# Kernel tuning notes

Hardware: AMD Instinct MI355X
Metric: run time of the kernel (lower is better)

Reference implementation:

```python
import jax, jax.numpy as jnp
from jax import lax
import numpy as np

B, S = 64, 16
GD, LD, PD, HD, CD = 64, 32, 8, 64, 64  # global, local, periodic, hidden, coder dims
TWO_PI = 6.283185307179586


def _conv(x, w, b):
    y = lax.conv_general_dilated(x, w, (2, 2), [(1, 1), (1, 1)])
    return y + b[None, :, None, None]


def _deconv(x, w, b):
    # torch ConvTranspose2d(k=4, s=2, p=1); w is [in, out, 4, 4].
    # Equivalent: dilate lhs by 2, pad k-1-p=2 each side, conv with flipped kernel.
    wt = jnp.flip(w, (2, 3)).transpose(1, 0, 2, 3)  # -> OIHW
    y = lax.conv_general_dilated(x, wt, (1, 1), [(2, 2), (2, 2)], lhs_dilation=(2, 2))
    return y + b[None, :, None, None]


def _bn(x, g, b, eps=1e-5):
    # training-mode BatchNorm2d (biased variance, per-channel affine)
    m = x.mean((0, 2, 3), keepdims=True)
    v = x.var((0, 2, 3), keepdims=True)
    return (x - m) * lax.rsqrt(v + eps) * g[None, :, None, None] + b[None, :, None, None]


def setup_inputs() -> dict:
    key = jax.random.key(0)
    ks = iter(jax.random.split(key, 40))
    n = lambda shape, s=0.02: jax.random.normal(next(ks), shape, jnp.float32) * s
    return {
        "Z_l": jax.random.normal(next(ks), (B, LD, S, S), jnp.float32),
        "Z_g": jax.random.normal(next(ks), (B, GD, S, S), jnp.float32),
        "imgs": jax.random.normal(next(ks), (B, 3, 128, 128), jnp.float32),
        "phi": jax.random.uniform(next(ks), (B, PD, 1, 1), jnp.float32),
        "lW": n((HD, GD)), "lb": n((HD,)),
        "l1W": n((PD, HD)), "l1b": n((PD,)),
        "l2W": n((PD, HD)), "l2b": n((PD,)),
        "cod_w0": n((64, 3, 4, 4)), "cod_b0": n((64,)),
        "cod_g0": 1.0 + n((64,)), "cod_be0": n((64,)),
        "cod_w1": n((128, 64, 4, 4)), "cod_b1": n((128,)),
        "cod_g1": 1.0 + n((128,)), "cod_be1": n((128,)),
        "cod_w2": n((CD, 128, 4, 4)), "cod_b2": n((CD,)),
        "gen_w0": n((CD + LD + GD + PD, 256, 4, 4)), "gen_b0": n((256,)),
        "gen_g0": 1.0 + n((256,)), "gen_be0": n((256,)),
        "gen_w1": n((256, 128, 4, 4)), "gen_b1": n((128,)),
        "gen_g1": 1.0 + n((128,)), "gen_be1": n((128,)),
        "gen_w2": n((128, 3, 4, 4)), "gen_b2": n((3,)),
    }


def reference(Z_l, Z_g, imgs, phi, lW, lb, l1W, l1b, l2W, l2b,
              cod_w0, cod_b0, cod_g0, cod_be0, cod_w1, cod_b1, cod_g1, cod_be1,
              cod_w2, cod_b2,
              gen_w0, gen_b0, gen_g0, gen_be0, gen_w1, gen_b1, gen_g1, gen_be1,
              gen_w2, gen_b2):
    # --- image coder: [B,3,128,128] -> [B,CD,16,16] ---
    h = jax.nn.leaky_relu(_bn(_conv(imgs, cod_w0, cod_b0), cod_g0, cod_be0), 0.2)
    h = jax.nn.leaky_relu(_bn(_conv(h, cod_w1, cod_b1), cod_g1, cod_be1), 0.2)
    Z_c = jnp.tanh(_conv(h, cod_w2, cod_b2))
    # --- periodic noise: vectorized outer-product replacing S*S python loop ---
    zg = Z_g[:, :, 0, 0]                       # [B, GD]
    x = jax.nn.relu(zg @ lW.T + lb)            # [B, HD]
    K1 = x @ l1W.T + l1b                       # [B, PD]
    K2 = x @ l2W.T + l2b                       # [B, PD]
    idx = jnp.arange(S, dtype=jnp.float32)
    wave = K1[:, :, None, None] * idx[:, None] + K2[:, :, None, None] * idx[None, :]
    Z_p = jnp.sin(wave + phi * TWO_PI)         # [B, PD, S, S]
    # --- generator ---
    Z = jnp.concatenate((Z_c, Z_l, Z_g, Z_p), axis=1)  # [B, 168, 16, 16]
    h = jax.nn.relu(_bn(_deconv(Z, gen_w0, gen_b0), gen_g0, gen_be0))
    h = jax.nn.relu(_bn(_deconv(h, gen_w1, gen_b1), gen_g1, gen_be1))
    return jnp.tanh(_deconv(h, gen_w2, gen_b2))        # [B, 3, 128, 128]
```

## Files before the change

kernel.cpp:

```cpp
#include <hip/hip_runtime.h>
#include <hip/hip_bf16.h>

#define TWO_PI_F 6.2831853071795864769f

typedef __attribute__((ext_vector_type(8))) __bf16 bf16x8;
typedef __attribute__((ext_vector_type(4))) float f32x4;

__device__ __forceinline__ float bf2f_raw(unsigned short u) {
    return __uint_as_float(((unsigned int)u) << 16);
}
__device__ __forceinline__ unsigned short f2bf(float f) {
    unsigned int u = __float_as_uint(f);
    unsigned int r = (u + 0x7FFFu + ((u >> 16) & 1u)) >> 16;
    return (unsigned short)r;
}
__device__ __forceinline__ float loadIn(const void* p, size_t i, bool f32) {
    return f32 ? ((const float*)p)[i] : bf2f_raw(((const unsigned short*)p)[i]);
}

__device__ __forceinline__ uint4 bn_fuse8(uint4 v, const float* __restrict__ sc,
                                          const float* __restrict__ sh, int c0, float slope) {
    unsigned short us[8];
    *(uint4*)us = v;
#pragma unroll
    for (int k = 0; k < 8; ++k) {
        float f = bf2f_raw(us[k]) * sc[c0 + k] + sh[c0 + k];
        f = f > 0.f ? f : slope * f;
        us[k] = f2bf(f);
    }
    return *(const uint4*)us;
}

static constexpr size_t OFF_WC0 = 0;
static constexpr size_t OFF_WG2 = 3072;
static constexpr size_t OFF_P   = 9216;
static constexpr size_t OFF_CB0 = OFF_P + 0;
static constexpr size_t OFF_CG0 = OFF_P + 64;
static constexpr size_t OFF_CBE0= OFF_P + 128;
static constexpr size_t OFF_CB1 = OFF_P + 192;
static constexpr size_t OFF_CG1 = OFF_P + 320;
static constexpr size_t OFF_CBE1= OFF_P + 448;
static constexpr size_t OFF_CB2 = OFF_P + 576;
static constexpr size_t OFF_GB0 = OFF_P + 640;
static constexpr size_t OFF_GG0 = OFF_P + 896;
static constexpr size_t OFF_GBE0= OFF_P + 1152;
static constexpr size_t OFF_GB1 = OFF_P + 1408;
static constexpr size_t OFF_GG1 = OFF_P + 1536;
static constexpr size_t OFF_GBE1= OFF_P + 1664;
static constexpr size_t OFF_GB2 = OFF_P + 1792;
static constexpr size_t OFF_SSUM  = OFF_P + 2048;
static constexpr size_t OFF_SSQ   = OFF_SSUM + 576;
static constexpr size_t OFF_SCALE = OFF_SSUM + 1152;
static constexpr size_t OFF_SHIFT = OFF_SCALE + 576;
static constexpr size_t OFF_K12   = OFF_SHIFT + 576;
static constexpr size_t OFF_FLAG  = OFF_K12 + 1024;
static constexpr size_t FP32_END  = OFF_FLAG + 16;
static constexpr size_t UXT = 2 * FP32_END;
static constexpr size_t UYT = UXT + 16777216;
static constexpr size_t UZT = UYT + 8388608;
static constexpr size_t UW0 = UYT + 33554432;
static constexpr size_t UW1 = UW0 + 786432;
static constexpr size_t UWC1 = UW1 + 524288;
static constexpr size_t UWC2 = UWC1 + 131072;
static constexpr size_t UW2 = UWC2 + 131072;
static constexpr size_t WS_END_USHORT = UW2 + 32768;
static constexpr size_t WS_NEED_BYTES = WS_END_USHORT * 2;


__global__ void detect_kernel(const unsigned short* __restrict__ imgs, int* __restrict__ flag) {
    int t = threadIdx.x;
    unsigned short u = imgs[t];
    int e = (u >> 7) & 0xFF;
    unsigned long long b = __ballot(e >= 0xC0);
    __shared__ int cnt[4];
    if ((t & 63) == 0) cnt[t >> 6] = __popcll(b);
    __syncthreads();
    if (t == 0) flag[0] = (cnt[0] + cnt[1] + cnt[2] + cnt[3] >= 4) ? 1 : 0;
}

struct CvtJobs {
    const void* src[16];
    float* dst[16];
    int off[17];
};

__global__ void cvt_all_kernel(CvtJobs J, int total, const int* __restrict__ flg) {
    int i = blockIdx.x * 256 + threadIdx.x;
    if (i >= total) return;
    bool f32 = flg[0] != 0;
    int k = 0;
#pragma unroll
    for (int t = 0; t < 15; ++t) { if (i >= J.off[t + 1]) k = t + 1; }
    int r = i - J.off[k];
    J.dst[k][r] = loadIn(J.src[k], r, f32);
}

__global__ void zero_kernel(float* p, int n) {
    int i = blockIdx.x * 256 + threadIdx.x;
    if (i < n) p[i] = 0.f;
}

__global__ void pack_w2_kernel(const void* __restrict__ src, unsigned short* __restrict__ dst,
                               int ICreal, int ICP, int OC, const int* __restrict__ flg) {
    bool f32 = flg[0] != 0;
    int i = blockIdx.x * 256 + threadIdx.x;
    int total = 16 * OC * ICP;
    if (i >= total) return;
    int jj = i & 7;
    int lane = (i >> 3) & 63;
    int j = (i >> 9) & 3;
    int t3 = i >> 11;
    int NK = ICP / 32;
    int kc = t3 % NK;
    int t4 = t3 / NK;
    int NOCT = OC / 64;
    int oct = t4 % NOCT;
    int ktap = t4 / NOCT;
    int kq = lane >> 4, n = lane & 15;
    int ic = kc * 32 + kq * 8 + jj;
    int oc = oct * 64 + n * 4 + j;
    unsigned short v = 0;
    if (ic < ICreal) v = f2bf(loadIn(src, ((size_t)(ic * OC + oc) << 4) + ktap, f32));
    dst[i] = v;
}

__global__ void pack_w2s_kernel(const void* __restrict__ src, unsigned short* __restrict__ dst,
                                int ICP, int OCreal, const int* __restrict__ flg) {
    bool f32 = flg[0] != 0;
    int i = blockIdx.x * 256 + threadIdx.x;
    int NK = ICP / 32;
    int total = 16 * NK * 512;
    if (i >= total) return;
    int jj = i & 7;
    int lane = (i >> 3) & 63;
    int t3 = i >> 9;
    int kc = t3 % NK;
    int ktap = t3 / NK;
    int kq = lane >> 4, n = lane & 15;
    int ic = kc * 32 + kq * 8 + jj;
    unsigned short v = 0;
    if (n < OCreal) v = f2bf(loadIn(src, ((size_t)(ic * OCreal + n) << 4) + ktap, f32));
    dst[i] = v;
}

__global__ void pack_wc_kernel(const void* __restrict__ src, unsigned short* __restrict__ dst,
                               int IC, int OC, const int* __restrict__ flg) {
    bool f32 = flg[0] != 0;
    int i = blockIdx.x * 256 + threadIdx.x;
    int total = 16 * OC * IC;
    if (i >= total) return;
    int jj = i & 7;
    int lane = (i >> 3) & 63;
    int j = (i >> 9) & 3;
    int t3 = i >> 11;
    int NK = IC / 32;
    int kc = t3 % NK;
    int t4 = t3 / NK;
    int NOCT = OC / 64;
    int oct = t4 % NOCT;
    int ktap = t4 / NOCT;
    int kq = lane >> 4, n = lane & 15;
    int ic = kc * 32 + kq * 8 + jj;
    int oc = oct * 64 + j * 16 + n;
    dst[i] = f2bf(loadIn(src, ((size_t)(oc * IC + ic) << 4) + ktap, f32));
}

__global__ void mlp_kernel(const void* __restrict__ Zg,
                           const void* __restrict__ lW, const void* __restrict__ lb,
                           const void* __restrict__ l1W, const void* __restrict__ l1b,
                           const void* __restrict__ l2W, const void* __restrict__ l2b,
                           float* __restrict__ K12, const int* __restrict__ flg) {
    bool f32 = flg[0] != 0;
    int b = blockIdx.x;
    int t = threadIdx.x;
    __shared__ float xs[64];
    float acc = loadIn(lb, t, f32);
    for (int c = 0; c < 64; ++c)
        acc += loadIn(Zg, (size_t)(b * 64 + c) * 256, f32) * loadIn(lW, t * 64 + c, f32);
    xs[t] = fmaxf(acc, 0.f);
    __syncthreads();
    if (t < 16) {
        int p = t & 7;
        const void* Wp = (t < 8) ? l1W : l2W;
        const void* bp = (t < 8) ? l1b : l2b;
        float a = loadIn(bp, p, f32);
        for (int h = 0; h < 64; ++h) a += xs[h] * loadIn(Wp, p * 64 + h, f32);
        K12[b * 16 + t] = a;
    }
}

__global__ void conv0_s2d_kernel(const void* __restrict__ imgs, const float* __restrict__ w,
                                 const float* __restrict__ bias, unsigned short* __restrict__ xs,
                                 const int* __restrict__ flg) {
    bool f32 = flg[0] != 0;
    int b = blockIdx.z;
    int tile = blockIdx.x;
    int Y0 = (tile >> 2) * 16, X0 = (tile & 3) * 16;
    __shared__ float vin[3 * 34 * 35];
    __shared__ float wl[64 * 49];
    for (int i = threadIdx.x; i < 3 * 34 * 34; i += 256) {
        int c = i % 34; int t = i / 34; int r = t % 34; int ic = t / 34;
        int iy = 2 * Y0 - 1 + r, ix = 2 * X0 - 1 + c;
        float v = 0.f;
        if (((unsigned)iy < 128u) & ((unsigned)ix < 128u))
            v = loadIn(imgs, ((size_t)(b * 3 + ic) * 128 + iy) * 128 + ix, f32);
        vin[(ic * 34 + r) * 35 + c] = v;
    }
    for (int i = threadIdx.x; i < 3072; i += 256) {
        int oc = i / 48, idx = i % 48;
        wl[oc * 49 + idx] = w[i];
    }
    __syncthreads();
    int q = threadIdx.x >> 2;
    int ocq = threadIdx.x & 3;
    int qy = q >> 3, qx = q & 7;
    float acc[4][16];
#pragma unroll
    for (int p = 0; p < 4; ++p)
#pragma unroll
        for (int o = 0; o < 16; ++o) acc[p][o] = 0.f;
    for (int ic = 0; ic < 3; ++ic) {
        float v[6][6];
#pragma unroll
        for (int r = 0; r < 6; ++r)
#pragma unroll
            for (int c = 0; c < 6; ++c)
                v[r][c] = vin[(ic * 34 + 4 * qy + r) * 35 + 4 * qx + c];
#pragma unroll
        for (int o = 0; o < 16; ++o) {
            const float* wo = wl + (ocq * 16 + o) * 49 + ic * 16;
#pragma unroll
            for (int ky = 0; ky < 4; ++ky)
#pragma unroll
                for (int kx = 0; kx < 4; ++kx) {
                    float wv = wo[ky * 4 + kx];
                    acc[0][o] = fmaf(v[ky][kx], wv, acc[0][o]);
                    acc[1][o] = fmaf(v[ky][kx + 2], wv, acc[1][o]);
                    acc[2][o] = fmaf(v[ky + 2][kx], wv, acc[2][o]);
                    acc[3][o] = fmaf(v[ky + 2][kx + 2], wv, acc[3][o]);
                }
        }
    }
    int j = (Y0 >> 1) + qy, i2 = (X0 >> 1) + qx;
#pragma unroll
    for (int p = 0; p < 4; ++p) {
        int dy = p >> 1, dx = p & 1;
        unsigned short tmp[16];
#pragma unroll
        for (int o = 0; o < 16; ++o) tmp[o] = f2bf(acc[p][o] + bias[ocq * 16 + o]);
        unsigned short* dst = xs + (((size_t)((b * 2 + dy) * 2 + dx) * 32 + j) * 32 + i2) * 64 + ocq * 16;
        *(uint4*)(dst) = *(const uint4*)(tmp);
        *(uint4*)(dst + 8) = *(const uint4*)(tmp + 8);
    }
}

__global__ void conv1_mfma_kernel(const unsigned short* __restrict__ xs,
                                  const unsigned short* __restrict__ wp,
                                  const float* __restrict__ bias,
                                  const float* __restrict__ sc, const float* __restrict__ sh,
                                  unsigned short* __restrict__ ys) {
    constexpr int STR = 72;
    __shared__ unsigned short lds[4 * 3 * 17 * STR];
    int bid = blockIdx.x;
    int xt = bid & 1;
    int qp = (bid >> 1) & 15;
    int b = bid >> 5;
    int oy0 = qp * 2, x0 = xt * 16;
    for (int i = threadIdx.x; i < 1632; i += 256) {
        int icc = i & 7; int t = i >> 3;
        int col = t % 17; int rc = t / 17;
        int row = rc % 3; int pl = rc / 3;
        int py = pl >> 1, px = pl & 1;
        int j = oy0 - py + row;
        int ci = x0 - px + col;
        uint4 v = {0u, 0u, 0u, 0u};
        if (((unsigned)j < 32u) & ((unsigned)ci < 32u)) {
            v = *(const uint4*)(xs + ((size_t)((b * 4 + pl) * 32 + j) * 32 + ci) * 64 + icc * 8);
            v = bn_fuse8(v, sc, sh, icc * 8, 0.2f);
        }
        *(uint4*)(lds + ((pl * 3 + row) * 17 + col) * STR + icc * 8) = v;
    }
    __syncthreads();

    int wv = threadIdx.x >> 6, lane = threadIdx.x & 63;
    int r = wv >> 1, oct = wv & 1;
    int m = lane & 15, kq = lane >> 4;
    f32x4 acc[4];
#pragma unroll
    for (int j = 0; j < 4; ++j) acc[j] = (f32x4){0.f, 0.f, 0.f, 0.f};

#pragma unroll
    for (int ky = 0; ky < 4; ++ky) {
        int py = (ky & 1) ^ 1;
        int lrow = r + (ky >> 1);
#pragma unroll
        for (int kx = 0; kx < 4; ++kx) {
            int px = (kx & 1) ^ 1;
            int pl = py * 2 + px;
            int lcol = m + (kx >> 1);
            const unsigned short* lp = lds + ((pl * 3 + lrow) * 17 + lcol) * STR + kq * 8;
            int ktap = ky * 4 + kx;
            const unsigned short* bb = wp + (size_t)(ktap * 2 + oct) * 4096;
#pragma unroll
            for (int kc = 0; kc < 2; ++kc) {
                bf16x8 a = *(const bf16x8*)(lp + kc * 32);
                const unsigned short* bk = bb + kc * 2048 + lane * 8;
                bf16x8 b0 = *(const bf16x8*)(bk);
                bf16x8 b1 = *(const bf16x8*)(bk + 512);
                bf16x8 b2 = *(const bf16x8*)(bk + 1024);
                bf16x8 b3 = *(const bf16x8*)(bk + 1536);
                acc[0] = __builtin_amdgcn_mfma_f32_16x16x32_bf16(a, b0, acc[0], 0, 0, 0);
                acc[1] = __builtin_amdgcn_mfma_f32_16x16x32_bf16(a, b1, acc[1], 0, 0, 0);
                acc[2] = __builtin_amdgcn_mfma_f32_16x16x32_bf16(a, b2, acc[2], 0, 0, 0);
                acc[3] = __builtin_amdgcn_mfma_f32_16x16x32_bf16(a, b3, acc[3], 0, 0, 0);
            }
        }
    }
    int oy = oy0 + r;
    int pyo = oy & 1, jo = oy >> 1;
    int n = m;
    float bv0 = bias[oct * 64 + n], bv1 = bias[oct * 64 + 16 + n];
    float bv2 = bias[oct * 64 + 32 + n], bv3 = bias[oct * 64 + 48 + n];
#pragma unroll
    for (int reg = 0; reg < 4; ++reg) {
        int mm = kq * 4 + reg;
        int ox = x0 + mm;
        int pxo = ox & 1, io = ox >> 1;
        size_t base = (((size_t)((b * 2 + pyo) * 2 + pxo) * 16 + jo) * 16 + io) * 128 + oct * 64 + n;
        ys[base]      = f2bf(acc[0][reg] + bv0);
        ys[base + 16] = f2bf(acc[1][reg] + bv1);
        ys[base + 32] = f2bf(acc[2][reg] + bv2);
        ys[base + 48] = f2bf(acc[3][reg] + bv3);
    }
}

__global__ void conv2_mfma_kernel(const unsigned short* __restrict__ ys,
                                  const unsigned short* __restrict__ wp,
                                  const float* __restrict__ bias,
                                  const float* __restrict__ sc, const float* __restrict__ sh,
                                  unsigned short* __restrict__ zt) {
    constexpr int STR = 136;
    __shared__ unsigned short lds[4 * 3 * 17 * STR];
    int bid = blockIdx.x;
    int qp = bid & 7;
    int b = bid >> 3;
    int oy0 = qp * 2;
    for (int i = threadIdx.x; i < 3264; i += 256) {
        int icc = i & 15; int t = i >> 4;
        int col = t % 17; int rc = t / 17;
        int row = rc % 3; int pl = rc / 3;
        int py = pl >> 1, px = pl & 1;
        int j = oy0 - py + row;
        int ci = col - px;
        uint4 v = {0u, 0u, 0u, 0u};
        if (((unsigned)j < 16u) & ((unsigned)ci < 16u)) {
            v = *(const uint4*)(ys + ((size_t)((b * 4 + pl) * 16 + j) * 16 + ci) * 128 + icc * 8);
            v = bn_fuse8(v, sc, sh, icc * 8, 0.2f);
        }
        *(uint4*)(lds + ((pl * 3 + row) * 17 + col) * STR + icc * 8) = v;
    }
    __syncthreads();

    int wv = threadIdx.x >> 6, lane = threadIdx.x & 63;
    int r = wv >> 1, jh = wv & 1;
    int m = lane & 15, kq = lane >> 4;
    f32x4 acc[2];
    acc[0] = (f32x4){0.f, 0.f, 0.f, 0.f};
    acc[1] = acc[0];
#pragma unroll
    for (int ky = 0; ky < 4; ++ky) {
        int py = (ky & 1) ^ 1;
        int lrow = r + (ky >> 1);
#pragma unroll
        for (int kx = 0; kx < 4; ++kx) {
            int px = (kx & 1) ^ 1;
            int pl = py * 2 + px;
            int lcol = m + (kx >> 1);
            const unsigned short* lp = lds + ((pl * 3 + lrow) * 17 + lcol) * STR + kq * 8;
            int ktap = ky * 4 + kx;
            const unsigned short* bb = wp + (size_t)ktap * 8192;
#pragma unroll
            for (int kc = 0; kc < 4; ++kc) {
                bf16x8 a = *(const bf16x8*)(lp + kc * 32);
                const unsigned short* bk = bb + kc * 2048 + (jh * 2) * 512 + lane * 8;
                bf16x8 b0 = *(const bf16x8*)(bk);
                bf16x8 b1 = *(const bf16x8*)(bk + 512);
                acc[0] = __builtin_amdgcn_mfma_f32_16x16x32_bf16(a, b0, acc[0], 0, 0, 0);
                acc[1] = __builtin_amdgcn_mfma_f32_16x16x32_bf16(a, b1, acc[1], 0, 0, 0);
            }
        }
    }
    int oy = oy0 + r;
    int n = m;
    float bv0 = bias[(jh * 2) * 16 + n], bv1 = bias[(jh * 2 + 1) * 16 + n];
#pragma unroll
    for (int reg = 0; reg < 4; ++reg) {
        int x = kq * 4 + reg;
        size_t base = ((size_t)(b * 16 + oy) * 16 + x) * 192 + (jh * 2) * 16 + n;
        zt[base]      = f2bf(tanhf(acc[0][reg] + bv0));
        zt[base + 16] = f2bf(tanhf(acc[1][reg] + bv1));
    }
}

__global__ void assemble_z(const void* __restrict__ Zl, const void* __restrict__ Zg,
                           const void* __restrict__ phi, const float* __restrict__ K12,
                           unsigned short* __restrict__ zt, const int* __restrict__ flg) {
    bool f32 = flg[0] != 0;
    int i = blockIdx.x * 256 + threadIdx.x;
    const int TOT = 64 * 104 * 256;
    if (i >= TOT) return;
    int pos = i & 255;
    int t = i >> 8;
    int c104 = t % 104;
    int b = t / 104;
    float val;
    if (c104 < 32) {
        val = loadIn(Zl, ((size_t)(b * 32 + c104) << 8) + pos, f32);
    } else if (c104 < 96) {
        val = loadIn(Zg, ((size_t)(b * 64 + (c104 - 32)) << 8) + pos, f32);
    } else {
        int p = c104 - 96;
        int y = pos >> 4, x = pos & 15;
        float k1 = K12[b * 16 + p];
        float k2 = K12[b * 16 + 8 + p];
        val = sinf(k1 * (float)y + k2 * (float)x + loadIn(phi, b * 8 + p, f32) * TWO_PI_F);
    }
    zt[((size_t)(b * 256 + pos)) * 192 + 64 + c104] = f2bf(val);
}

template <int ICP, int Q, int OC, int QR, bool BN>
__global__ __launch_bounds__(256, 2)
void deconv_mfma2_kernel(const unsigned short* __restrict__ in_t,
                         const unsigned short* __restrict__ wp2,
                         const float* __restrict__ bias,
                         const float* __restrict__ sc, const float* __restrict__ sh,
                         unsigned short* __restrict__ out_t) {
    constexpr int NOCT = OC / 64;
    constexpr int NK = ICP / 32;
    constexpr int XT = Q / 16;
    constexpr int NQB = Q / QR;
    constexpr int ROWS = QR + 2;
    constexpr int STRIDE = ICP + 8;
    constexpr int NTILES = XT * NQB * 64;
    __shared__ unsigned short lds[ROWS * 18 * STRIDE];

    int bid = blockIdx.x;
    int oct = bid / NTILES;
    bid -= oct * NTILES;
    int xt = bid % XT;
    int t2 = bid / XT;
    int qp = t2 % NQB;
    int b = t2 / NQB;
    int qy0 = qp * QR;
    int x0 = xt * 16;

    constexpr int P8 = ICP / 8;
    constexpr int E8 = ROWS * 18 * P8;
    for (int i = threadIdx.x; i < E8; i += 256) {
        int icc = i % P8;
        int rc = i / P8;
        int row = rc / 18, col = rc % 18;
        int y = qy0 - 1 + row, x = x0 - 1 + col;
        uint4 val = {0u, 0u, 0u, 0u};
        if (((unsigned)y < (unsigned)Q) & ((unsigned)x < (unsigned)Q)) {
            val = *(const uint4*)(in_t + (size_t)((b * Q + y) * Q + x) * ICP + icc * 8);
            if (BN) val = bn_fuse8(val, sc, sh, icc * 8, 0.f);
        }
        *(uint4*)(lds + rc * STRIDE + icc * 8) = val;
    }
    __syncthreads();

    int wv = threadIdx.x >> 6, lane = threadIdx.x & 63;
    int dy = wv >> 1, dx = wv & 1;
    int m = lane & 15, kq = lane >> 4;

    f32x4 acc[QR][4];
#pragma unroll
    for (int q = 0; q < QR; ++q)
#pragma unroll
        for (int j = 0; j < 4; ++j) acc[q][j] = (f32x4){0.f, 0.f, 0.f, 0.f};

#pragma unroll
    for (int t = 0; t < 4; ++t) {
        int rr = t >> 1, cc = t & 1;
        int ktap = ((3 - dy) - 2 * rr) * 4 + ((3 - dx) - 2 * cc);
        int col = m + dx + cc;
        int row0 = dy + rr;
        const unsigned short* bbase = wp2 + (size_t)((ktap * NOCT + oct) * NK) * 2048;
#pragma unroll
        for (int kc = 0; kc < NK; ++kc) {
            bf16x8 a[QR];
#pragma unroll
            for (int q = 0; q < QR; ++q)
                a[q] = *(const bf16x8*)(lds + ((row0 + q) * 18 + col) * STRIDE + kc * 32 + kq * 8);
            bf16x8 b0 = *(const bf16x8*)(bbase + (kc * 4 + 0) * 512 + lane * 8);
            bf16x8 b1 = *(const bf16x8*)(bbase + (kc * 4 + 1) * 512 + lane * 8);
            bf16x8 b2 = *(const bf16x8*)(bbase + (kc * 4 + 2) * 512 + lane * 8);
            bf16x8 b3 = *(const bf16x8*)(bbase + (kc * 4 + 3) * 512 + lane * 8);
#pragma unroll
            for (int q = 0; q < QR; ++q) {
                acc[q][0] = __builtin_amdgcn_mfma_f32_16x16x32_bf16(a[q], b0, acc[q][0], 0, 0, 0);
                acc[q][1] = __builtin_amdgcn_mfma_f32_16x16x32_bf16(a[q], b1, acc[q][1], 0, 0, 0);
                acc[q][2] = __builtin_amdgcn_mfma_f32_16x16x32_bf16(a[q], b2, acc[q][2], 0, 0, 0);
                acc[q][3] = __builtin_amdgcn_mfma_f32_16x16x32_bf16(a[q], b3, acc[q][3], 0, 0, 0);
            }
        }
    }
    int n = m;
    const float4 bv = *(const float4*)(bias + oct * 64 + 4 * n);
#pragma unroll
    for (int qyl = 0; qyl < QR; ++qyl) {
        int oy = 2 * (qy0 + qyl) + dy;
#pragma unroll
        for (int reg = 0; reg < 4; ++reg) {
            int mm = kq * 4 + reg;
            int ox = 2 * (x0 + mm) + dx;
            size_t base = ((size_t)((b * 2 * Q + oy) * (2 * Q) + ox)) * OC + oct * 64 + 4 * n;
            ushort4 tv;
            tv.x = f2bf(acc[qyl][0][reg] + bv.x);
            tv.y = f2bf(acc[qyl][1][reg] + bv.y);
            tv.z = f2bf(acc[qyl][2][reg] + bv.z);
            tv.w = f2bf(acc[qyl][3][reg] + bv.w);
            *(ushort4*)(out_t + base) = tv;
        }
    }
}

__global__ void deconv2_mfma_kernel(const unsigned short* __restrict__ yt,
                                    const unsigned short* __restrict__ wp,
                                    const float* __restrict__ bias,
                                    const float* __restrict__ sc, const float* __restrict__ sh,
                                    float* __restrict__ outp) {
    constexpr int Q = 64, ICP = 128, NK = 4, STRIDE = 136;
    __shared__ unsigned short lds[4 * 18 * STRIDE];
    int bid = blockIdx.x;
    int xt = bid & 3;
    int t2 = bid >> 2;
    int qp = t2 & 31;
    int b = t2 >> 5;
    int qy0 = qp * 2, x0 = xt * 16;

    for (int i = threadIdx.x; i < 4 * 18 * 16; i += 256) {
        int icc = i & 15;
        int rc = i >> 4;
        int row = rc / 18, col = rc % 18;
        int y = qy0 - 1 + row, x = x0 - 1 + col;
        uint4 v = {0u, 0u, 0u, 0u};
        if (((unsigned)y < (unsigned)Q) & ((unsigned)x < (unsigned)Q)) {
            v = *(const uint4*)(yt + (size_t)((b * Q + y) * Q + x) * ICP + icc * 8);
            v = bn_fuse8(v, sc, sh, icc * 8, 0.f);
        }
        *(uint4*)(lds + rc * STRIDE + icc * 8) = v;
    }
    __syncthreads();

    int wv = threadIdx.x >> 6, lane = threadIdx.x & 63;
    int dy = wv >> 1, dx = wv & 1;
    int m = lane & 15, kq = lane >> 4;
    f32x4 acc0 = {0.f, 0.f, 0.f, 0.f}, acc1 = acc0;

#pragma unroll
    for (int t = 0; t < 4; ++t) {
        int rr = t >> 1, cc = t & 1;
        int ktap = ((3 - dy) - 2 * rr) * 4 + ((3 - dx) - 2 * cc);
        int col = m + dx + cc;
        int row0 = dy + rr;
        const unsigned short* bb = wp + (size_t)(ktap * NK) * 512;
#pragma unroll
        for (int kc = 0; kc < NK; ++kc) {
            bf16x8 a0 = *(const bf16x8*)(lds + (row0 * 18 + col) * STRIDE + kc * 32 + kq * 8);
            bf16x8 a1 = *(const bf16x8*)(lds + ((row0 + 1) * 18 + col) * STRIDE + kc * 32 + kq * 8);
            bf16x8 b0 = *(const bf16x8*)(bb + kc * 512 + lane * 8);
            acc0 = __builtin_amdgcn_mfma_f32_16x16x32_bf16(a0, b0, acc0, 0, 0, 0);
            acc1 = __builtin_amdgcn_mfma_f32_16x16x32_bf16(a1, b0, acc1, 0, 0, 0);
        }
    }
    int n = m;
    if (n < 3) {
        float bv = bias[n];
#pragma unroll
        for (int reg = 0; reg < 4; ++reg) {
            int mm = kq * 4 + reg;
            int ox = 2 * (x0 + mm) + dx;
            int oy0_ = 2 * qy0 + dy;
            size_t ob = (size_t)(b * 3 + n) * 16384;
            outp[ob + (size_t)oy0_ * 128 + ox]       = tanhf(acc0[reg] + bv);
            outp[ob + (size_t)(oy0_ + 2) * 128 + ox] = tanhf(acc1[reg] + bv);
        }
    }
}

template <int C>
__global__ void stat_reduce_t(const unsigned short* __restrict__ x, int total4,
                              float* __restrict__ ssum, float* __restrict__ ssq, int statoff) {
    __shared__ float ls[C], lq[C];
    for (int c = threadIdx.x; c < C; c += 256) { ls[c] = 0.f; lq[c] = 0.f; }
    __syncthreads();
    int i0 = blockIdx.x * 256 + threadIdx.x;
    int stride = gridDim.x * 256;
    int c0 = (i0 << 2) & (C - 1);
    float s0 = 0, s1 = 0, s2 = 0, s3 = 0, q0 = 0, q1 = 0, q2 = 0, q3 = 0;
    for (int i = i0; i < total4; i += stride) {
        ushort4 v = *(const ushort4*)(x + ((size_t)i << 2));
        float f0 = bf2f_raw(v.x), f1 = bf2f_raw(v.y), f2 = bf2f_raw(v.z), f3 = bf2f_raw(v.w);
        s0 += f0; s1 += f1; s2 += f2; s3 += f3;
        q0 += f0 * f0; q1 += f1 * f1; q2 += f2 * f2; q3 += f3 * f3;
    }
    atomicAdd(&ls[c0], s0); atomicAdd(&ls[c0 + 1], s1); atomicAdd(&ls[c0 + 2], s2); atomicAdd(&ls[c0 + 3], s3);
    atomicAdd(&lq[c0], q0); atomicAdd(&lq[c0 + 1], q1); atomicAdd(&lq[c0 + 2], q2); atomicAdd(&lq[c0 + 3], q3);
    __syncthreads();
    for (int c = threadIdx.x; c < C; c += 256) {
        atomicAdd(&ssum[statoff + c], ls[c]);
        atomicAdd(&ssq[statoff + c], lq[c]);
    }
}

__global__ void bn_fin_kernel(const float* __restrict__ ssum, const float* __restrict__ ssq,
                              const float* __restrict__ g, const float* __restrict__ be,
                              float* __restrict__ scale, float* __restrict__ shift,
                              int statoff, int C, float invN) {
    int c = threadIdx.x;
    if (c >= C) return;
    float m = ssum[statoff + c] * invN;
    float v = ssq[statoff + c] * invN - m * m;
    v = fmaxf(v, 0.f);
    float sc = g[c] * rsqrtf(v + 1e-5f);
    scale[statoff + c] = sc;
    shift[statoff + c] = be[c] - m * sc;
}

extern "C" void kernel_launch(void* const* d_in, const int* in_sizes, int n_in,
                              void* d_out, int out_size, void* d_ws, size_t ws_size,
                              hipStream_t stream) {
    if (ws_size < WS_NEED_BYTES) {
        hipMemsetAsync(d_out, 0, (size_t)out_size * 4, stream);
        return;
    }

    float* W = (float*)d_ws;
    unsigned short* U = (unsigned short*)d_ws;
    int* FLG = (int*)(W + OFF_FLAG);

    detect_kernel<<<1, 256, 0, stream>>>((const unsigned short*)d_in[2], FLG);

    CvtJobs J;
    const int srcIdx[16] = {10, 28, 11, 12, 13, 15, 16, 17, 19, 21, 22, 23, 25, 26, 27, 29};
    const int cnt[16]    = {3072, 6144, 64, 64, 64, 128, 128, 128, 64, 256, 256, 256, 128, 128, 128, 3};
    float* dsts[16] = {W + OFF_WC0, W + OFF_WG2,
                       W + OFF_CB0, W + OFF_CG0, W + OFF_CBE0, W + OFF_CB1, W + OFF_CG1, W + OFF_CBE1,
                       W + OFF_CB2, W + OFF_GB0, W + OFF_GG0, W + OFF_GBE0, W + OFF_GB1, W + OFF_GG1,
                       W + OFF_GBE1, W + OFF_GB2};
    int off = 0;
    for (int k = 0; k < 16; ++k) {
        J.src[k] = d_in[srcIdx[k]];
        J.dst[k] = dsts[k];
        J.off[k] = off;
        off += cnt[k];
    }
    J.off[16] = off;
    cvt_all_kernel<<<(off + 255) / 256, 256, 0, stream>>>(J, off, FLG);

    zero_kernel<<<5, 256, 0, stream>>>(W + OFF_SSUM, 1152);
    zero_kernel<<<6144, 256, 0, stream>>>((float*)(U + UZT), 1572864);

    pack_w2_kernel<<<3072, 256, 0, stream>>>(d_in[20], U + UW0, 168, 192, 256, FLG);
    pack_w2_kernel<<<2048, 256, 0, stream>>>(d_in[24], U + UW1, 256, 256, 128, FLG);
    pack_wc_kernel<<<512, 256, 0, stream>>>(d_in[14], U + UWC1, 64, 128, FLG);
    pack_wc_kernel<<<512, 256, 0, stream>>>(d_in[18], U + UWC2, 128, 64, FLG);
    pack_w2s_kernel<<<128, 256, 0, stream>>>(d_in[28], U + UW2, 128, 3, FLG);

    mlp_kernel<<<64, 64, 0, stream>>>(d_in[1], d_in[4], d_in[5], d_in[6], d_in[7],
                                      d_in[8], d_in[9], W + OFF_K12, FLG);

    conv0_s2d_kernel<<<dim3(16, 1, 64), 256, 0, stream>>>(d_in[2], W + OFF_WC0, W + OFF_CB0,
                                                          U + UXT, FLG);
    stat_reduce_t<64><<<1024, 256, 0, stream>>>(U + UXT, 4194304, W + OFF_SSUM, W + OFF_SSQ, 0);
    bn_fin_kernel<<<1, 256, 0, stream>>>(W + OFF_SSUM, W + OFF_SSQ, W + OFF_CG0, W + OFF_CBE0,
                                         W + OFF_SCALE, W + OFF_SHIFT, 0, 64, 1.f / 262144.f);

    conv1_mfma_kernel<<<2048, 256, 0, stream>>>(U + UXT, U + UWC1, W + OFF_CB1,
                                                W + OFF_SCALE + 0, W + OFF_SHIFT + 0, U + UYT);
    stat_reduce_t<128><<<1024, 256, 0, stream>>>(U + UYT, 2097152, W + OFF_SSUM, W + OFF_SSQ, 64);
    bn_fin_kernel<<<1, 256, 0, stream>>>(W + OFF_SSUM, W + OFF_SSQ, W + OFF_CG1, W + OFF_CBE1,
                                         W + OFF_SCALE, W + OFF_SHIFT, 64, 128, 1.f / 65536.f);

    conv2_mfma_kernel<<<512, 256, 0, stream>>>(U + UYT, U + UWC2, W + OFF_CB2,
                                               W + OFF_SCALE + 64, W + OFF_SHIFT + 64, U + UZT);

    assemble_z<<<6656, 256, 0, stream>>>(d_in[0], d_in[1], d_in[3], W + OFF_K12, U + UZT, FLG);

    deconv_mfma2_kernel<192, 16, 256, 4, false><<<1024, 256, 0, stream>>>(
        U + UZT, U + UW0, W + OFF_GB0, nullptr, nullptr, U + UXT);
    stat_reduce_t<256><<<1024, 256, 0, stream>>>(U + UXT, 4194304, W + OFF_SSUM, W + OFF_SSQ, 192);
    bn_fin_kernel<<<1, 256, 0, stream>>>(W + OFF_SSUM, W + OFF_SSQ, W + OFF_GG0, W + OFF_GBE0,
                                         W + OFF_SCALE, W + OFF_SHIFT, 192, 256, 1.f / 65536.f);

    deconv_mfma2_kernel<256, 32, 128, 4, true><<<2048, 256, 0, stream>>>(
        U + UXT, U + UW1, W + OFF_GB1, W + OFF_SCALE + 192, W + OFF_SHIFT + 192, U + UYT);
    stat_reduce_t<128><<<1024, 256, 0, stream>>>(U + UYT, 8388608, W + OFF_SSUM, W + OFF_SSQ, 448);
    bn_fin_kernel<<<1, 256, 0, stream>>>(W + OFF_SSUM, W + OFF_SSQ, W + OFF_GG1, W + OFF_GBE1,
                                         W + OFF_SCALE, W + OFF_SHIFT, 448, 128, 1.f / 262144.f);

    deconv2_mfma_kernel<<<8192, 256, 0, stream>>>(U + UYT, U + UW2, W + OFF_GB2,
                                                  W + OFF_SCALE + 448, W + OFF_SHIFT + 448,
                                                  (float*)d_out);
}
```

Before: 694.6 us.

## Fuse BatchNorm statistics into conv/deconv epilogues and drop separate reductions

The conv1 and both deconv kernels now accumulate per-channel sum and sum-of-squares in their epilogues. They combine these through LDS atomics and then global atomics, which removes three stat_reduce passes that re-read the bf16 activations. assemble_z now also writes zeros into the padding channels, so the full zero-fill of the Z buffer is dropped. The deconvs switch QR from 4 to 2, double the grid and raise launch bounds to 4 blocks per CU. The stats are computed from the fp32 values before bf16 rounding, and the global float atomics make the reduction order nondeterministic.

```diff
diff --git a/kernel.cpp b/kernel.cpp
--- a/kernel.cpp
+++ b/kernel.cpp
@@ -258,9 +258,11 @@
                                   const unsigned short* __restrict__ wp,
                                   const float* __restrict__ bias,
                                   const float* __restrict__ sc, const float* __restrict__ sh,
+                                  float* __restrict__ gsum, float* __restrict__ gsq,
                                   unsigned short* __restrict__ ys) {
     constexpr int STR = 72;
     __shared__ unsigned short lds[4 * 3 * 17 * STR];
+    __shared__ float cs[128], cq[128];
     int bid = blockIdx.x;
     int xt = bid & 1;
     int qp = (bid >> 1) & 15;
@@ -280,6 +282,7 @@
         }
         *(uint4*)(lds + ((pl * 3 + row) * 17 + col) * STR + icc * 8) = v;
     }
+    if (threadIdx.x < 128) { cs[threadIdx.x] = 0.f; cq[threadIdx.x] = 0.f; }
     __syncthreads();
 
     int wv = threadIdx.x >> 6, lane = threadIdx.x & 63;
@@ -321,16 +324,30 @@
     int n = m;
     float bv0 = bias[oct * 64 + n], bv1 = bias[oct * 64 + 16 + n];
     float bv2 = bias[oct * 64 + 32 + n], bv3 = bias[oct * 64 + 48 + n];
+    float s0 = 0, s1 = 0, s2 = 0, s3 = 0, q0 = 0, q1 = 0, q2 = 0, q3 = 0;
 #pragma unroll
     for (int reg = 0; reg < 4; ++reg) {
         int mm = kq * 4 + reg;
         int ox = x0 + mm;
         int pxo = ox & 1, io = ox >> 1;
         size_t base = (((size_t)((b * 2 + pyo) * 2 + pxo) * 16 + jo) * 16 + io) * 128 + oct * 64 + n;
-        ys[base]      = f2bf(acc[0][reg] + bv0);
-        ys[base + 16] = f2bf(acc[1][reg] + bv1);
-        ys[base + 32] = f2bf(acc[2][reg] + bv2);
-        ys[base + 48] = f2bf(acc[3][reg] + bv3);
+        float v0 = acc[0][reg] + bv0, v1 = acc[1][reg] + bv1;
+        float v2 = acc[2][reg] + bv2, v3 = acc[3][reg] + bv3;
+        s0 += v0; q0 += v0 * v0; s1 += v1; q1 += v1 * v1;
+        s2 += v2; q2 += v2 * v2; s3 += v3; q3 += v3 * v3;
+        ys[base]      = f2bf(v0);
+        ys[base + 16] = f2bf(v1);
+        ys[base + 32] = f2bf(v2);
+        ys[base + 48] = f2bf(v3);
+    }
+    atomicAdd(&cs[oct * 64 + n], s0);      atomicAdd(&cq[oct * 64 + n], q0);
+    atomicAdd(&cs[oct * 64 + 16 + n], s1); atomicAdd(&cq[oct * 64 + 16 + n], q1);
+    atomicAdd(&cs[oct * 64 + 32 + n], s2); atomicAdd(&cq[oct * 64 + 32 + n], q2);
+    atomicAdd(&cs[oct * 64 + 48 + n], s3); atomicAdd(&cq[oct * 64 + 48 + n], q3);
+    __syncthreads();
+    if (threadIdx.x < 128) {
+        atomicAdd(&gsum[64 + threadIdx.x], cs[threadIdx.x]);
+        atomicAdd(&gsq[64 + threadIdx.x], cq[threadIdx.x]);
     }
 }
 
@@ -407,33 +424,36 @@
                            unsigned short* __restrict__ zt, const int* __restrict__ flg) {
     bool f32 = flg[0] != 0;
     int i = blockIdx.x * 256 + threadIdx.x;
-    const int TOT = 64 * 104 * 256;
+    const int TOT = 64 * 128 * 256;
     if (i >= TOT) return;
     int pos = i & 255;
     int t = i >> 8;
-    int c104 = t % 104;
-    int b = t / 104;
+    int c128 = t % 128;
+    int b = t / 128;
     float val;
-    if (c104 < 32) {
-        val = loadIn(Zl, ((size_t)(b * 32 + c104) << 8) + pos, f32);
-    } else if (c104 < 96) {
-        val = loadIn(Zg, ((size_t)(b * 64 + (c104 - 32)) << 8) + pos, f32);
-    } else {
-        int p = c104 - 96;
+    if (c128 < 32) {
+        val = loadIn(Zl, ((size_t)(b * 32 + c128) << 8) + pos, f32);
+    } else if (c128 < 96) {
+        val = loadIn(Zg, ((size_t)(b * 64 + (c128 - 32)) << 8) + pos, f32);
+    } else if (c128 < 104) {
+        int p = c128 - 96;
         int y = pos >> 4, x = pos & 15;
         float k1 = K12[b * 16 + p];
         float k2 = K12[b * 16 + 8 + p];
         val = sinf(k1 * (float)y + k2 * (float)x + loadIn(phi, b * 8 + p, f32) * TWO_PI_F);
-    }
-    zt[((size_t)(b * 256 + pos)) * 192 + 64 + c104] = f2bf(val);
-}
-
-template <int ICP, int Q, int OC, int QR, bool BN>
-__global__ __launch_bounds__(256, 2)
+    } else {
+        val = 0.f;
+    }
+    zt[((size_t)(b * 256 + pos)) * 192 + 64 + c128] = f2bf(val);
+}
+
+template <int ICP, int Q, int OC, int QR, bool BN, bool ST>
+__global__ __launch_bounds__(256, 4)
 void deconv_mfma2_kernel(const unsigned short* __restrict__ in_t,
                          const unsigned short* __restrict__ wp2,
                          const float* __restrict__ bias,
                          const float* __restrict__ sc, const float* __restrict__ sh,
+                         float* __restrict__ gsum, float* __restrict__ gsq, int statoff,
                          unsigned short* __restrict__ out_t) {
     constexpr int NOCT = OC / 64;
     constexpr int NK = ICP / 32;
@@ -443,6 +463,7 @@
     constexpr int STRIDE = ICP + 8;
     constexpr int NTILES = XT * NQB * 64;
     __shared__ unsigned short lds[ROWS * 18 * STRIDE];
+    __shared__ float sstat[64], qstat[64];
 
     int bid = blockIdx.x;
     int oct = bid / NTILES;
@@ -468,6 +489,7 @@
         }
         *(uint4*)(lds + rc * STRIDE + icc * 8) = val;
     }
+    if (ST && threadIdx.x < 64) { sstat[threadIdx.x] = 0.f; qstat[threadIdx.x] = 0.f; }
     __syncthreads();
 
     int wv = threadIdx.x >> 6, lane = threadIdx.x & 63;
@@ -508,6 +530,7 @@
     }
     int n = m;
     const float4 bv = *(const float4*)(bias + oct * 64 + 4 * n);
+    float s0 = 0, s1 = 0, s2 = 0, s3 = 0, q0 = 0, q1 = 0, q2 = 0, q3 = 0;
 #pragma unroll
     for (int qyl = 0; qyl < QR; ++qyl) {
         int oy = 2 * (qy0 + qyl) + dy;
@@ -516,12 +539,28 @@
             int mm = kq * 4 + reg;
             int ox = 2 * (x0 + mm) + dx;
             size_t base = ((size_t)((b * 2 * Q + oy) * (2 * Q) + ox)) * OC + oct * 64 + 4 * n;
+            float v0 = acc[qyl][0][reg] + bv.x;
+            float v1 = acc[qyl][1][reg] + bv.y;
+            float v2 = acc[qyl][2][reg] + bv.z;
+            float v3 = acc[qyl][3][reg] + bv.w;
+            if (ST) {
+                s0 += v0; q0 += v0 * v0; s1 += v1; q1 += v1 * v1;
+                s2 += v2; q2 += v2 * v2; s3 += v3; q3 += v3 * v3;
+            }
             ushort4 tv;
-            tv.x = f2bf(acc[qyl][0][reg] + bv.x);
-            tv.y = f2bf(acc[qyl][1][reg] + bv.y);
-            tv.z = f2bf(acc[qyl][2][reg] + bv.z);
-            tv.w = f2bf(acc[qyl][3][reg] + bv.w);
+            tv.x = f2bf(v0); tv.y = f2bf(v1); tv.z = f2bf(v2); tv.w = f2bf(v3);
             *(ushort4*)(out_t + base) = tv;
+        }
+    }
+    if (ST) {
+        atomicAdd(&sstat[4 * n + 0], s0); atomicAdd(&qstat[4 * n + 0], q0);
+        atomicAdd(&sstat[4 * n + 1], s1); atomicAdd(&qstat[4 * n + 1], q1);
+        atomicAdd(&sstat[4 * n + 2], s2); atomicAdd(&qstat[4 * n + 2], q2);
+        atomicAdd(&sstat[4 * n + 3], s3); atomicAdd(&qstat[4 * n + 3], q3);
+        __syncthreads();
+        if (threadIdx.x < 64) {
+            atomicAdd(&gsum[statoff + oct * 64 + threadIdx.x], sstat[threadIdx.x]);
+            atomicAdd(&gsq[statoff + oct * 64 + threadIdx.x], qstat[threadIdx.x]);
         }
     }
 }
@@ -661,7 +700,6 @@
     cvt_all_kernel<<<(off + 255) / 256, 256, 0, stream>>>(J, off, FLG);
 
     zero_kernel<<<5, 256, 0, stream>>>(W + OFF_SSUM, 1152);
-    zero_kernel<<<6144, 256, 0, stream>>>((float*)(U + UZT), 1572864);
 
     pack_w2_kernel<<<3072, 256, 0, stream>>>(d_in[20], U + UW0, 168, 192, 256, FLG);
     pack_w2_kernel<<<2048, 256, 0, stream>>>(d_in[24], U + UW1, 256, 256, 128, FLG);
@@ -679,25 +717,25 @@
                                          W + OFF_SCALE, W + OFF_SHIFT, 0, 64, 1.f / 262144.f);
 
     conv1_mfma_kernel<<<2048, 256, 0, stream>>>(U + UXT, U + UWC1, W + OFF_CB1,
-                                                W + OFF_SCALE + 0, W + OFF_SHIFT + 0, U + UYT);
-    stat_reduce_t<128><<<1024, 256, 0, stream>>>(U + UYT, 2097152, W + OFF_SSUM, W + OFF_SSQ, 64);
+                                                W + OFF_SCALE + 0, W + OFF_SHIFT + 0,
+                                                W + OFF_SSUM, W + OFF_SSQ, U + UYT);
     bn_fin_kernel<<<1, 256, 0, stream>>>(W + OFF_SSUM, W + OFF_SSQ, W + OFF_CG1, W + OFF_CBE1,
                                          W + OFF_SCALE, W + OFF_SHIFT, 64, 128, 1.f / 65536.f);
 
     conv2_mfma_kernel<<<512, 256, 0, stream>>>(U + UYT, U + UWC2, W + OFF_CB2,
                                                W + OFF_SCALE + 64, W + OFF_SHIFT + 64, U + UZT);
 
-    assemble_z<<<6656, 256, 0, stream>>>(d_in[0], d_in[1], d_in[3], W + OFF_K12, U + UZT, FLG);
-
-    deconv_mfma2_kernel<192, 16, 256, 4, false><<<1024, 256, 0, stream>>>(
-        U + UZT, U + UW0, W + OFF_GB0, nullptr, nullptr, U + UXT);
-    stat_reduce_t<256><<<1024, 256, 0, stream>>>(U + UXT, 4194304, W + OFF_SSUM, W + OFF_SSQ, 192);
+    assemble_z<<<8192, 256, 0, stream>>>(d_in[0], d_in[1], d_in[3], W + OFF_K12, U + UZT, FLG);
+
+    deconv_mfma2_kernel<192, 16, 256, 2, false, true><<<2048, 256, 0, stream>>>(
+        U + UZT, U + UW0, W + OFF_GB0, nullptr, nullptr,
+        W + OFF_SSUM, W + OFF_SSQ, 192, U + UXT);
     bn_fin_kernel<<<1, 256, 0, stream>>>(W + OFF_SSUM, W + OFF_SSQ, W + OFF_GG0, W + OFF_GBE0,
                                          W + OFF_SCALE, W + OFF_SHIFT, 192, 256, 1.f / 65536.f);
 
-    deconv_mfma2_kernel<256, 32, 128, 4, true><<<2048, 256, 0, stream>>>(
-        U + UXT, U + UW1, W + OFF_GB1, W + OFF_SCALE + 192, W + OFF_SHIFT + 192, U + UYT);
-    stat_reduce_t<128><<<1024, 256, 0, stream>>>(U + UYT, 8388608, W + OFF_SSUM, W + OFF_SSQ, 448);
+    deconv_mfma2_kernel<256, 32, 128, 2, true, true><<<4096, 256, 0, stream>>>(
+        U + UXT, U + UW1, W + OFF_GB1, W + OFF_SCALE + 192, W + OFF_SHIFT + 192,
+        W + OFF_SSUM, W + OFF_SSQ, 448, U + UYT);
     bn_fin_kernel<<<1, 256, 0, stream>>>(W + OFF_SSUM, W + OFF_SSQ, W + OFF_GG1, W + OFF_GBE1,
                                          W + OFF_SCALE, W + OFF_SHIFT, 448, 128, 1.f / 262144.f);
 
```

Result: no change. 683.2 us (-1.6%).
